# Performance work log

Measured on AMD Instinct MI355X. Metric: run time of the kernel, lower is better.

## Reference

```python
import jax, jax.numpy as jnp
import numpy as np
from jax.ops import segment_sum

N_NODES = 100000
N_EDGES = 1600000
HIDDEN = 64
N_LAYERS = 4
N_CLASSES = 10
N_GRAPHS = 512


def setup_inputs() -> dict:
    key = jax.random.key(0)
    ks = jax.random.split(key, 9)
    x = jax.random.normal(ks[0], (N_NODES, HIDDEN), dtype=jnp.float32)
    edge_index = jax.random.randint(ks[1], (2, N_EDGES), 0, N_NODES, dtype=jnp.int32)
    batch = jnp.sort(jax.random.randint(ks[2], (N_NODES,), 0, N_GRAPHS, dtype=jnp.int32))
    s = 0.05
    W_enc = jax.random.normal(ks[3], (HIDDEN, HIDDEN), dtype=jnp.float32) * s
    b_enc = jax.random.normal(ks[4], (HIDDEN,), dtype=jnp.float32) * s
    W_conv = jax.random.normal(ks[5], (N_LAYERS, HIDDEN, HIDDEN), dtype=jnp.float32) * s
    b_conv = jax.random.normal(ks[6], (N_LAYERS, HIDDEN), dtype=jnp.float32) * s
    W_out = jax.random.normal(ks[7], (HIDDEN, N_CLASSES), dtype=jnp.float32) * s
    b_out = jax.random.normal(ks[8], (N_CLASSES,), dtype=jnp.float32) * s
    return {"x": x, "edge_index": edge_index, "batch": batch,
            "W_enc": W_enc, "b_enc": b_enc, "W_conv": W_conv, "b_conv": b_conv,
            "W_out": W_out, "b_out": b_out, "num_graphs": N_GRAPHS}


def reference(x, edge_index, batch, W_enc, b_enc, W_conv, b_conv, W_out, b_out, num_graphs):
    N = x.shape[0]
    src, dst = edge_index[0], edge_index[1]
    # atom_encoder: Linear
    h = x @ W_enc + b_enc
    # GCN symmetric normalization with self-loops (PyG GCNConv default):
    # deg counts incoming edges (dst) plus the self-loop.
    deg = segment_sum(jnp.ones_like(src, dtype=h.dtype), dst, num_segments=N) + 1.0
    deg_inv_sqrt = jax.lax.rsqrt(deg)
    deg_inv = 1.0 / deg  # self-loop norm = d^-1/2 * d^-1/2
    edge_norm = (deg_inv_sqrt[src] * deg_inv_sqrt[dst])[:, None]  # [E,1]
    for l in range(W_conv.shape[0]):
        hl = h @ W_conv[l]                          # [N,H]
        msg = hl[src] * edge_norm                   # gather + normalize [E,H]
        agg = segment_sum(msg, dst, num_segments=N) # scatter-add
        h = agg + hl * deg_inv[:, None] + b_conv[l] # self-loop + bias
        h = jax.nn.silu(h)                          # dropout p=0 / eval: identity
    # global_add_pool over graph ids
    pooled = segment_sum(h, batch, num_segments=num_graphs)  # [G,H]
    # readout: Linear + ReLU (make_mlp with hidden_layers=1)
    out = jax.nn.relu(pooled @ W_out + b_out)
    return out
```

## Files before the change

### kernel.cpp

```cpp
#include <hip/hip_runtime.h>
#include <math.h>

#define HIDDEN 64
#define N_LAYERS 4
#define N_CLASSES 10
#define N_GRAPHS 512
#define BSH 8
#define NPB 256
#define PART_K 2048
#define IDX_CAP 512

typedef _Float16 __h;
typedef __attribute__((ext_vector_type(8))) _Float16 half8;
typedef __attribute__((ext_vector_type(4))) float f32x4;

__global__ __launch_bounds__(256) void k_histA(const int* __restrict__ dst,
                                               int* __restrict__ ghist, int E, int NB) {
    __shared__ int hist[512];
    int t = threadIdx.x;
    hist[t] = 0; hist[t + 256] = 0;
    __syncthreads();
    int base = blockIdx.x * PART_K;
    int kend = min(PART_K, E - base);
    for (int k = t; k < kend; k += 256) atomicAdd(&hist[dst[base + k] >> BSH], 1);
    __syncthreads();
    for (int j = t; j < NB; j += 256) {
        int h = hist[j];
        if (h) atomicAdd(&ghist[j], h);
    }
}

__global__ __launch_bounds__(256) void k_bucketscan(const int* __restrict__ ghist,
                                                    int* __restrict__ bucketbase,
                                                    int* __restrict__ gcur, int NB) {
    __shared__ int s[256];
    int t = threadIdx.x;
    int j0 = 2 * t, j1 = 2 * t + 1;
    int h0 = (j0 < NB) ? ghist[j0] : 0;
    int h1 = (j1 < NB) ? ghist[j1] : 0;
    s[t] = h0 + h1; __syncthreads();
    for (int o = 1; o < 256; o <<= 1) {
        int x = (t >= o) ? s[t - o] : 0;
        __syncthreads();
        s[t] += x;
        __syncthreads();
    }
    int base = (t == 0) ? 0 : s[t - 1];
    if (j0 <= NB) { bucketbase[j0] = base;      gcur[j0] = base; }
    if (j1 <= NB) { bucketbase[j1] = base + h0; gcur[j1] = base + h0; }
}

__global__ __launch_bounds__(256) void k_partition(const int* __restrict__ src,
                                                   const int* __restrict__ dst,
                                                   int* __restrict__ gcur,
                                                   int* __restrict__ packed,
                                                   int E, int NB) {
    __shared__ int hist[512];
    __shared__ int scanE[512];
    __shared__ int cur[512];
    __shared__ int delta[512];
    __shared__ int ps[256];
    __shared__ int stage[PART_K];
    __shared__ unsigned short stgj[PART_K];
    int t = threadIdx.x;
    int base = blockIdx.x * PART_K;
    int kend = min(PART_K, E - base);

    hist[t] = 0; hist[t + 256] = 0;
    __syncthreads();
    for (int k = t; k < kend; k += 256) atomicAdd(&hist[dst[base + k] >> BSH], 1);
    __syncthreads();

    int j0 = 2 * t, j1 = j0 + 1;
    int h0 = hist[j0], h1 = hist[j1];
    ps[t] = h0 + h1; __syncthreads();
    for (int o = 1; o < 256; o <<= 1) {
        int x = (t >= o) ? ps[t - o] : 0;
        __syncthreads();
        ps[t] += x;
        __syncthreads();
    }
    int bexc = (t == 0) ? 0 : ps[t - 1];
    scanE[j0] = bexc;
    scanE[j1] = bexc + h0;
    __syncthreads();

    for (int j = t; j < NB; j += 256) {
        int h = hist[j];
        int g = h ? atomicAdd(&gcur[j], h) : 0;
        delta[j] = g - scanE[j];
        cur[j]   = scanE[j];
    }
    __syncthreads();

    for (int k = t; k < kend; k += 256) {
        int d = dst[base + k], s = src[base + k];
        int j = d >> BSH;
        int pos = atomicAdd(&cur[j], 1);
        stage[pos] = (s << BSH) | (d & (NPB - 1));
        stgj[pos]  = (unsigned short)j;
    }
    __syncthreads();

    for (int i = t; i < kend; i += 256) {
        packed[i + delta[stgj[i]]] = stage[i];
    }
}

__global__ __launch_bounds__(256) void k_fill3(const int* __restrict__ packed,
                                               const int* __restrict__ bucketbase,
                                               int* __restrict__ rowptr,
                                               float* __restrict__ dis,
                                               int* __restrict__ csr_src,
                                               int N, int E) {
    __shared__ int cnt[256];
    __shared__ int rp[256];
    int j = blockIdx.x;
    int t = threadIdx.x;
    int node0 = j << BSH;
    int segb = bucketbase[j];
    int sege = bucketbase[j + 1];

    cnt[t] = 0; __syncthreads();
    for (int i = segb + t; i < sege; i += 256) atomicAdd(&cnt[packed[i] & (NPB - 1)], 1);
    __syncthreads();

    int c = cnt[t];
    rp[t] = c; __syncthreads();
    for (int o = 1; o < 256; o <<= 1) {
        int x = (t >= o) ? rp[t - o] : 0;
        __syncthreads();
        rp[t] += x;
        __syncthreads();
    }
    int node = node0 + t;
    int start = segb + rp[t] - c + node;
    if (node < N) {
        rowptr[node] = start;
        dis[node] = rsqrtf((float)c + 1.0f);
        csr_src[start] = node;
        if (node == N - 1) rowptr[N] = E + N;
    }
    __syncthreads();
    cnt[t] = start + 1;
    __syncthreads();
    for (int i = segb + t; i < sege; i += 256) {
        int v = packed[i];
        int slot = atomicAdd(&cnt[v & (NPB - 1)], 1);
        csr_src[slot] = v >> BSH;
    }
}

__device__ __forceinline__ half8 shfl_xor_h8(half8 v, int m) {
    int4 u = __builtin_bit_cast(int4, v);
    u.x = __shfl_xor(u.x, m);
    u.y = __shfl_xor(u.y, m);
    u.z = __shfl_xor(u.z, m);
    u.w = __shfl_xor(u.w, m);
    return __builtin_bit_cast(half8, u);
}

__global__ __launch_bounds__(256) void k_prepW(const float* __restrict__ Wconv,
                                               const float* __restrict__ Wenc,
                                               __h* __restrict__ Wh) {
    int idx = blockIdx.x * 256 + threadIdx.x;
    int l = idx >> 12;
    int kn = idx & 4095;
    int k = kn >> 6, n = kn & 63;
    int nt = n >> 4, nl = n & 15;
    int kt = k >> 5, kr = k & 31;
    int quad = kr >> 3, j = kr & 7;
    int lane = quad * 16 + nl;
    int pos = (((nt * 2 + kt) * 64 + lane) << 3) + j;
    float w = (l < N_LAYERS) ? Wconv[(size_t)l * 4096 + kn] : Wenc[kn];
    Wh[(l << 12) + pos] = (__h)w;
}

__global__ __launch_bounds__(256) void k_layer(const int* __restrict__ csr_src,
                                               const int* __restrict__ rowptr,
                                               const float* __restrict__ dis,
                                               const __h* __restrict__ G,
                                               const __h* __restrict__ Wh,
                                               const float* __restrict__ bias,
                                               const int* __restrict__ batch,
                                               __h* __restrict__ Gho,
                                               float* __restrict__ pooled,
                                               int N, int last) {
    __shared__ __attribute__((aligned(16))) __h At[16][72];
    __shared__ int sidx[IDX_CAP];
    int tid  = threadIdx.x;
    int wave = tid >> 6;
    int lane = tid & 63;
    int trow0 = blockIdx.x * 16;
    int g16 = lane >> 4;
    int sub = (lane >> 3) & 1;
    int f8  = lane & 7;
    unsigned f8b = (unsigned)f8 * 16u;

    int rpi = trow0 + lane;
    int rpv = rowptr[rpi > N ? N : rpi];
    int beg0 = __shfl(rpv, 0);
    int endL = __shfl(rpv, 16);
    int L    = endL - beg0;
    bool fits = (L <= IDX_CAP);

    if (fits) {
        const int* __restrict__ gsrc = csr_src + beg0;
        for (int k = tid; k < L; k += 256) sidx[k] = gsrc[k];
    }
    __syncthreads();

    int i   = wave * 4 + g16;
    int beg = __shfl(rpv, i);
    int end = __shfl(rpv, i + 1);
    int node = trow0 + i;

    const char* Gb = (const char*)G;
    const half8 z8 = {(__h)0.f, (__h)0.f, (__h)0.f, (__h)0.f,
                      (__h)0.f, (__h)0.f, (__h)0.f, (__h)0.f};
    half8 a = z8;
#define GLOAD(s) (*(const half8*)(Gb + ((((unsigned)(s)) << 7) + f8b)))

    if (fits) {
        const int* sp = sidx;
        int rb = beg - beg0, re = end - beg0;
        for (int e = rb + sub * 8; e < re; e += 16) {
            if (e + 8 <= re) {
                int s0 = sp[e + 0], s1 = sp[e + 1], s2 = sp[e + 2], s3 = sp[e + 3];
                int s4 = sp[e + 4], s5 = sp[e + 5], s6 = sp[e + 6], s7 = sp[e + 7];
                half8 r0 = GLOAD(s0), r1 = GLOAD(s1), r2 = GLOAD(s2), r3 = GLOAD(s3);
                half8 r4 = GLOAD(s4), r5 = GLOAD(s5), r6 = GLOAD(s6), r7 = GLOAD(s7);
                a += r0; a += r1; a += r2; a += r3;
                a += r4; a += r5; a += r6; a += r7;
            } else {
                #pragma unroll
                for (int k = 0; k < 8; ++k) {
                    int ek = e + k;
                    int ck = ek < re ? ek : re - 1;
                    half8 r = GLOAD(sp[ck]);
                    a += (ek < re) ? r : z8;
                }
            }
        }
    } else {
        for (int e = beg + sub * 8; e < end; e += 16) {
            if (e + 8 <= end) {
                int s0 = csr_src[e + 0], s1 = csr_src[e + 1], s2 = csr_src[e + 2], s3 = csr_src[e + 3];
                int s4 = csr_src[e + 4], s5 = csr_src[e + 5], s6 = csr_src[e + 6], s7 = csr_src[e + 7];
                half8 r0 = GLOAD(s0), r1 = GLOAD(s1), r2 = GLOAD(s2), r3 = GLOAD(s3);
                half8 r4 = GLOAD(s4), r5 = GLOAD(s5), r6 = GLOAD(s6), r7 = GLOAD(s7);
                a += r0; a += r1; a += r2; a += r3;
                a += r4; a += r5; a += r6; a += r7;
            } else {
                #pragma unroll
                for (int k = 0; k < 8; ++k) {
                    int ek = e + k;
                    int ck = ek < end ? ek : end - 1;
                    half8 r = GLOAD(csr_src[ck]);
                    a += (ek < end) ? r : z8;
                }
            }
        }
    }
#undef GLOAD

    a += shfl_xor_h8(a, 8);

    if (sub == 0) {
        float df = (node < N) ? dis[node] : 0.0f;
        __h dd = (__h)df;
        half8 dv = {dd, dd, dd, dd, dd, dd, dd, dd};
        *(half8*)&At[i][f8 * 8] = a * dv;
    }
    __syncthreads();

    int quad = lane >> 4, nl = lane & 15;
    half8 bf[4][2];
    #pragma unroll
    for (int nt = 0; nt < 4; ++nt)
        #pragma unroll
        for (int kt = 0; kt < 2; ++kt)
            bf[nt][kt] = *(const half8*)(Wh + (((nt * 2 + kt) * 64 + lane) << 3));

    half8 a0 = *(const half8*)&At[nl][quad * 8];
    half8 a1 = *(const half8*)&At[nl][32 + quad * 8];

    f32x4 acc[4];
    #pragma unroll
    for (int nt = 0; nt < 4; ++nt) {
        acc[nt] = (f32x4){0.f, 0.f, 0.f, 0.f};
        acc[nt] = __builtin_amdgcn_mfma_f32_16x16x32_f16(a0, bf[nt][0], acc[nt], 0, 0, 0);
        acc[nt] = __builtin_amdgcn_mfma_f32_16x16x32_f16(a1, bf[nt][1], acc[nt], 0, 0, 0);
    }

    float b[4];
    #pragma unroll
    for (int nt = 0; nt < 4; ++nt) b[nt] = bias[nt * 16 + nl];

    bool own = (quad == wave);

    if (!last) {
        if (own) {
            #pragma unroll
            for (int reg = 0; reg < 4; ++reg) {
                int rr = trow0 + quad * 4 + reg;
                if (rr < N) {
                    float ds_ = dis[rr];
                    #pragma unroll
                    for (int nt = 0; nt < 4; ++nt) {
                        float v = acc[nt][reg] + b[nt];
                        v = v / (1.0f + expf(-v));
                        Gho[(size_t)rr * 64 + nt * 16 + nl] = (__h)(ds_ * v);
                    }
                }
            }
        }
    } else {
        if (own) {
            float run[4] = {0.f, 0.f, 0.f, 0.f};
            int cur = -1;
            #pragma unroll
            for (int reg = 0; reg < 4; ++reg) {
                int rr = trow0 + quad * 4 + reg;
                if (rr < N) {
                    int bi = batch[rr];
                    float vals[4];
                    #pragma unroll
                    for (int nt = 0; nt < 4; ++nt) {
                        float v = acc[nt][reg] + b[nt];
                        vals[nt] = v / (1.0f + expf(-v));
                    }
                    if (bi != cur) {
                        if (cur >= 0) {
                            #pragma unroll
                            for (int nt = 0; nt < 4; ++nt)
                                atomicAdd(&pooled[cur * 64 + nt * 16 + nl], run[nt]);
                        }
                        cur = bi;
                        #pragma unroll
                        for (int nt = 0; nt < 4; ++nt) run[nt] = vals[nt];
                    } else {
                        #pragma unroll
                        for (int nt = 0; nt < 4; ++nt) run[nt] += vals[nt];
                    }
                }
            }
            if (cur >= 0) {
                #pragma unroll
                for (int nt = 0; nt < 4; ++nt)
                    atomicAdd(&pooled[cur * 64 + nt * 16 + nl], run[nt]);
            }
        }
    }
}

__global__ __launch_bounds__(256) void k_gemm_mfma(const float* __restrict__ xf,
                                                   const __h* __restrict__ Wh,
                                                   const float* __restrict__ bias,
                                                   const float* __restrict__ dis,
                                                   __h* __restrict__ Gho,
                                                   int N) {
    int wave = threadIdx.x >> 6;
    int lane = threadIdx.x & 63;
    int row0 = (blockIdx.x * 4 + wave) * 32;
    if (row0 >= N) return;
    int quad = lane >> 4, nl = lane & 15;

    half8 bf[4][2];
    #pragma unroll
    for (int nt = 0; nt < 4; ++nt)
        #pragma unroll
        for (int kt = 0; kt < 2; ++kt)
            bf[nt][kt] = *(const half8*)(Wh + (((nt * 2 + kt) * 64 + lane) << 3));

    f32x4 acc[2][4];
    #pragma unroll
    for (int h = 0; h < 2; ++h) {
        int r = row0 + h * 16 + nl; if (r >= N) r = N - 1;
        const float* ap = xf + (size_t)r * 64 + quad * 8;
        float4 v0 = ((const float4*)ap)[0];
        float4 v1 = ((const float4*)ap)[1];
        float4 v2 = ((const float4*)(ap + 32))[0];
        float4 v3 = ((const float4*)(ap + 32))[1];
        half8 a0 = (half8){(__h)v0.x, (__h)v0.y, (__h)v0.z, (__h)v0.w,
                           (__h)v1.x, (__h)v1.y, (__h)v1.z, (__h)v1.w};
        half8 a1 = (half8){(__h)v2.x, (__h)v2.y, (__h)v2.z, (__h)v2.w,
                           (__h)v3.x, (__h)v3.y, (__h)v3.z, (__h)v3.w};
        #pragma unroll
        for (int nt = 0; nt < 4; ++nt) {
            acc[h][nt] = (f32x4){0.f, 0.f, 0.f, 0.f};
            acc[h][nt] = __builtin_amdgcn_mfma_f32_16x16x32_f16(a0, bf[nt][0], acc[h][nt], 0, 0, 0);
            acc[h][nt] = __builtin_amdgcn_mfma_f32_16x16x32_f16(a1, bf[nt][1], acc[h][nt], 0, 0, 0);
        }
    }

    float b[4];
    #pragma unroll
    for (int nt = 0; nt < 4; ++nt) b[nt] = bias[nt * 16 + nl];

    #pragma unroll
    for (int h = 0; h < 2; ++h) {
        #pragma unroll
        for (int reg = 0; reg < 4; ++reg) {
            int rr = row0 + h * 16 + quad * 4 + reg;
            if (rr < N) {
                float ds = dis[rr];
                #pragma unroll
                for (int nt = 0; nt < 4; ++nt) {
                    float v = acc[h][nt][reg] + b[nt];
                    Gho[(size_t)rr * 64 + nt * 16 + nl] = (__h)(ds * v);
                }
            }
        }
    }
}

__global__ __launch_bounds__(256) void k_readout(const float* __restrict__ pooled,
                                                 const float* __restrict__ Wout,
                                                 const float* __restrict__ bout,
                                                 float* __restrict__ out) {
    int idx = blockIdx.x * 256 + threadIdx.x;
    if (idx >= N_GRAPHS * N_CLASSES) return;
    int g = idx / N_CLASSES, c = idx % N_CLASSES;
    float s = bout[c];
    #pragma unroll
    for (int j = 0; j < 64; ++j) s += pooled[g * 64 + j] * Wout[j * N_CLASSES + c];
    out[idx] = fmaxf(s, 0.0f);
}

extern "C" void kernel_launch(void* const* d_in, const int* in_sizes, int n_in,
                              void* d_out, int out_size, void* d_ws, size_t ws_size,
                              hipStream_t stream) {
    const float* x      = (const float*)d_in[0];
    const int*   ei     = (const int*)d_in[1];
    const int*   batch  = (const int*)d_in[2];
    const float* W_enc  = (const float*)d_in[3];
    const float* b_enc  = (const float*)d_in[4];
    const float* W_conv = (const float*)d_in[5];
    const float* b_conv = (const float*)d_in[6];
    const float* W_out  = (const float*)d_in[7];
    const float* b_out  = (const float*)d_in[8];
    float* out = (float*)d_out;

    const int N = in_sizes[2];
    const int E = in_sizes[1] / 2;
    const int* src = ei;
    const int* dst = ei + E;
    const int NB   = (N + NPB - 1) >> BSH;
    const int NBLK = (E + PART_K - 1) / PART_K;

    char* ws = (char*)d_ws;
    size_t off = 0;
    auto alloc = [&](size_t bytes) -> char* {
        char* p = ws + off;
        off += (bytes + 255) & ~(size_t)255;
        return p;
    };
    int*   ghist      = (int*)alloc((size_t)(NB + 1) * sizeof(int));
    int*   bucketbase = (int*)alloc((size_t)(NB + 1) * sizeof(int));
    int*   gcur       = (int*)alloc((size_t)(NB + 1) * sizeof(int));
    int*   packed     = (int*)alloc((size_t)E * sizeof(int));
    int*   csr_src    = (int*)alloc((size_t)(E + N) * sizeof(int));
    int*   rowptr     = (int*)alloc((size_t)(N + 1) * sizeof(int));
    float* dis        = (float*)alloc((size_t)N * sizeof(float));
    __h*   bufA       = (__h*)alloc((size_t)N * HIDDEN * sizeof(__h));
    __h*   bufB       = (__h*)alloc((size_t)N * HIDDEN * sizeof(__h));
    __h*   Wh         = (__h*)alloc((size_t)(N_LAYERS + 1) * 4096 * sizeof(__h));
    float* pooled     = (float*)alloc((size_t)N_GRAPHS * HIDDEN * sizeof(float));
    (void)ws_size;

    hipMemsetAsync(ghist, 0, (size_t)(NB + 1) * sizeof(int), stream);
    hipMemsetAsync(pooled, 0, (size_t)N_GRAPHS * HIDDEN * sizeof(float), stream);

    k_histA     <<<NBLK, 256, 0, stream>>>(dst, ghist, E, NB);
    k_bucketscan<<<1,    256, 0, stream>>>(ghist, bucketbase, gcur, NB);
    k_partition <<<NBLK, 256, 0, stream>>>(src, dst, gcur, packed, E, NB);
    k_fill3     <<<NB,   256, 0, stream>>>(packed, bucketbase, rowptr, dis, csr_src, N, E);
    k_prepW<<<((N_LAYERS + 1) * 4096) / 256, 256, 0, stream>>>(W_conv, W_enc, Wh);

    int gb32 = (N + 127) / 128;
    k_gemm_mfma<<<gb32, 256, 0, stream>>>(x, Wh + (size_t)N_LAYERS * 4096, b_enc,
                                          dis, bufA, N);

    __h* bufs[2] = {bufA, bufB};
    int glayer = (N + 15) / 16;
    for (int l = 0; l < N_LAYERS; ++l) {
        int last = (l == N_LAYERS - 1);
        k_layer<<<glayer, 256, 0, stream>>>(csr_src, rowptr, dis, bufs[l & 1],
                                            Wh + (size_t)l * 4096,
                                            b_conv + (size_t)l * HIDDEN, batch,
                                            bufs[(l + 1) & 1], pooled, N, last);
    }

    k_readout<<<(N_GRAPHS * N_CLASSES + 255) / 256, 256, 0, stream>>>(pooled, W_out, b_out, out);
}
```

Measured before the change: 356.4 us.

## Make layer kernel persistent and pre-scale CSR source indices to byte offsets

The per-layer aggregation+MFMA kernel becomes a grid-stride persistent kernel capped at 2048 blocks. Weight fragments and bias are loaded once per block instead of once per 16-row tile. CSR source indices are stored pre-multiplied by the row byte stride, which removes a shift from each gather address. The gather also splits its sums across two accumulators for more ILP and uses a simpler guarded tail. The goal is lower launch, setup and address overhead, at the cost of less latency hiding from many resident blocks.

```diff
diff --git a/kernel.cpp b/kernel.cpp
--- a/kernel.cpp
+++ b/kernel.cpp
@@ -9,6 +9,7 @@
 #define NPB 256
 #define PART_K 2048
 #define IDX_CAP 512
+#define PBLK 2048
 
 typedef _Float16 __h;
 typedef __attribute__((ext_vector_type(8))) _Float16 half8;
@@ -138,7 +139,7 @@
     if (node < N) {
         rowptr[node] = start;
         dis[node] = rsqrtf((float)c + 1.0f);
-        csr_src[start] = node;
+        csr_src[start] = node << 7;
         if (node == N - 1) rowptr[N] = E + N;
     }
     __syncthreads();
@@ -147,7 +148,7 @@
     for (int i = segb + t; i < sege; i += 256) {
         int v = packed[i];
         int slot = atomicAdd(&cnt[v & (NPB - 1)], 1);
-        csr_src[slot] = v >> BSH;
+        csr_src[slot] = (v >> BSH) << 7;
     }
 }
 
@@ -185,170 +186,166 @@
                                                const int* __restrict__ batch,
                                                __h* __restrict__ Gho,
                                                float* __restrict__ pooled,
-                                               int N, int last) {
+                                               int N, int last, int ntiles) {
     __shared__ __attribute__((aligned(16))) __h At[16][72];
     __shared__ int sidx[IDX_CAP];
     int tid  = threadIdx.x;
     int wave = tid >> 6;
     int lane = tid & 63;
-    int trow0 = blockIdx.x * 16;
     int g16 = lane >> 4;
     int sub = (lane >> 3) & 1;
     int f8  = lane & 7;
-    unsigned f8b = (unsigned)f8 * 16u;
-
-    int rpi = trow0 + lane;
-    int rpv = rowptr[rpi > N ? N : rpi];
-    int beg0 = __shfl(rpv, 0);
-    int endL = __shfl(rpv, 16);
-    int L    = endL - beg0;
-    bool fits = (L <= IDX_CAP);
-
-    if (fits) {
-        const int* __restrict__ gsrc = csr_src + beg0;
-        for (int k = tid; k < L; k += 256) sidx[k] = gsrc[k];
-    }
-    __syncthreads();
-
-    int i   = wave * 4 + g16;
-    int beg = __shfl(rpv, i);
-    int end = __shfl(rpv, i + 1);
-    int node = trow0 + i;
-
+    int f8b = f8 * 16;
+    int quad = lane >> 4, nl = lane & 15;
     const char* Gb = (const char*)G;
     const half8 z8 = {(__h)0.f, (__h)0.f, (__h)0.f, (__h)0.f,
                       (__h)0.f, (__h)0.f, (__h)0.f, (__h)0.f};
-    half8 a = z8;
-#define GLOAD(s) (*(const half8*)(Gb + ((((unsigned)(s)) << 7) + f8b)))
-
-    if (fits) {
-        const int* sp = sidx;
-        int rb = beg - beg0, re = end - beg0;
-        for (int e = rb + sub * 8; e < re; e += 16) {
-            if (e + 8 <= re) {
+
+    half8 bf[4][2];
+    #pragma unroll
+    for (int nt = 0; nt < 4; ++nt)
+        #pragma unroll
+        for (int kt = 0; kt < 2; ++kt)
+            bf[nt][kt] = *(const half8*)(Wh + (((nt * 2 + kt) * 64 + lane) << 3));
+    float b[4];
+    #pragma unroll
+    for (int nt = 0; nt < 4; ++nt) b[nt] = bias[nt * 16 + nl];
+
+    for (int tile = blockIdx.x; tile < ntiles; tile += gridDim.x) {
+        int trow0 = tile * 16;
+
+        int rpi = trow0 + lane;
+        int rpv = rowptr[rpi > N ? N : rpi];
+        int beg0 = __shfl(rpv, 0);
+        int endL = __shfl(rpv, 16);
+        int L    = endL - beg0;
+        bool fits = (L <= IDX_CAP);
+
+        if (fits) {
+            const int* __restrict__ gsrc = csr_src + beg0;
+            for (int k = tid; k < L; k += 256) sidx[k] = gsrc[k];
+        }
+        __syncthreads();
+
+        int i   = wave * 4 + g16;
+        int beg = __shfl(rpv, i);
+        int end = __shfl(rpv, i + 1);
+        int node = trow0 + i;
+
+        half8 a = z8, a2 = z8;
+#define GLOAD(sv) (*(const half8*)(Gb + (unsigned)((sv) + f8b)))
+        if (fits) {
+            const int* sp = sidx;
+            int rb = beg - beg0, re = end - beg0;
+            int e = rb + sub * 8;
+            for (; e + 8 <= re; e += 16) {
                 int s0 = sp[e + 0], s1 = sp[e + 1], s2 = sp[e + 2], s3 = sp[e + 3];
                 int s4 = sp[e + 4], s5 = sp[e + 5], s6 = sp[e + 6], s7 = sp[e + 7];
                 half8 r0 = GLOAD(s0), r1 = GLOAD(s1), r2 = GLOAD(s2), r3 = GLOAD(s3);
                 half8 r4 = GLOAD(s4), r5 = GLOAD(s5), r6 = GLOAD(s6), r7 = GLOAD(s7);
-                a += r0; a += r1; a += r2; a += r3;
-                a += r4; a += r5; a += r6; a += r7;
-            } else {
+                a += r0; a2 += r1; a += r2; a2 += r3;
+                a += r4; a2 += r5; a += r6; a2 += r7;
+            }
+            if (e < re) {
                 #pragma unroll
                 for (int k = 0; k < 8; ++k) {
                     int ek = e + k;
-                    int ck = ek < re ? ek : re - 1;
-                    half8 r = GLOAD(sp[ck]);
-                    a += (ek < re) ? r : z8;
-                }
-            }
-        }
-    } else {
-        for (int e = beg + sub * 8; e < end; e += 16) {
-            if (e + 8 <= end) {
+                    if (ek < re) { half8 r = GLOAD(sp[ek]); a += r; }
+                }
+            }
+        } else {
+            int e = beg + sub * 8;
+            for (; e + 8 <= end; e += 16) {
                 int s0 = csr_src[e + 0], s1 = csr_src[e + 1], s2 = csr_src[e + 2], s3 = csr_src[e + 3];
                 int s4 = csr_src[e + 4], s5 = csr_src[e + 5], s6 = csr_src[e + 6], s7 = csr_src[e + 7];
                 half8 r0 = GLOAD(s0), r1 = GLOAD(s1), r2 = GLOAD(s2), r3 = GLOAD(s3);
                 half8 r4 = GLOAD(s4), r5 = GLOAD(s5), r6 = GLOAD(s6), r7 = GLOAD(s7);
-                a += r0; a += r1; a += r2; a += r3;
-                a += r4; a += r5; a += r6; a += r7;
-            } else {
+                a += r0; a2 += r1; a += r2; a2 += r3;
+                a += r4; a2 += r5; a += r6; a2 += r7;
+            }
+            if (e < end) {
                 #pragma unroll
                 for (int k = 0; k < 8; ++k) {
                     int ek = e + k;
-                    int ck = ek < end ? ek : end - 1;
-                    half8 r = GLOAD(csr_src[ck]);
-                    a += (ek < end) ? r : z8;
-                }
-            }
-        }
-    }
+                    if (ek < end) { half8 r = GLOAD(csr_src[ek]); a += r; }
+                }
+            }
+        }
 #undef GLOAD
-
-    a += shfl_xor_h8(a, 8);
-
-    if (sub == 0) {
-        float df = (node < N) ? dis[node] : 0.0f;
-        __h dd = (__h)df;
-        half8 dv = {dd, dd, dd, dd, dd, dd, dd, dd};
-        *(half8*)&At[i][f8 * 8] = a * dv;
-    }
-    __syncthreads();
-
-    int quad = lane >> 4, nl = lane & 15;
-    half8 bf[4][2];
-    #pragma unroll
-    for (int nt = 0; nt < 4; ++nt)
+        a += a2;
+        a += shfl_xor_h8(a, 8);
+
+        if (sub == 0) {
+            float df = (node < N) ? dis[node] : 0.0f;
+            __h dd = (__h)df;
+            half8 dv = {dd, dd, dd, dd, dd, dd, dd, dd};
+            *(half8*)&At[i][f8 * 8] = a * dv;
+        }
+        __syncthreads();
+
+        half8 a0 = *(const half8*)&At[nl][quad * 8];
+        half8 a1 = *(const half8*)&At[nl][32 + quad * 8];
+
+        f32x4 acc[4];
         #pragma unroll
-        for (int kt = 0; kt < 2; ++kt)
-            bf[nt][kt] = *(const half8*)(Wh + (((nt * 2 + kt) * 64 + lane) << 3));
-
-    half8 a0 = *(const half8*)&At[nl][quad * 8];
-    half8 a1 = *(const half8*)&At[nl][32 + quad * 8];
-
-    f32x4 acc[4];
-    #pragma unroll
-    for (int nt = 0; nt < 4; ++nt) {
-        acc[nt] = (f32x4){0.f, 0.f, 0.f, 0.f};
-        acc[nt] = __builtin_amdgcn_mfma_f32_16x16x32_f16(a0, bf[nt][0], acc[nt], 0, 0, 0);
-        acc[nt] = __builtin_amdgcn_mfma_f32_16x16x32_f16(a1, bf[nt][1], acc[nt], 0, 0, 0);
-    }
-
-    float b[4];
-    #pragma unroll
-    for (int nt = 0; nt < 4; ++nt) b[nt] = bias[nt * 16 + nl];
-
-    bool own = (quad == wave);
-
-    if (!last) {
-        if (own) {
-            #pragma unroll
-            for (int reg = 0; reg < 4; ++reg) {
-                int rr = trow0 + quad * 4 + reg;
-                if (rr < N) {
-                    float ds_ = dis[rr];
+        for (int nt = 0; nt < 4; ++nt) {
+            acc[nt] = (f32x4){0.f, 0.f, 0.f, 0.f};
+            acc[nt] = __builtin_amdgcn_mfma_f32_16x16x32_f16(a0, bf[nt][0], acc[nt], 0, 0, 0);
+            acc[nt] = __builtin_amdgcn_mfma_f32_16x16x32_f16(a1, bf[nt][1], acc[nt], 0, 0, 0);
+        }
+
+        bool own = (quad == wave);
+        if (!last) {
+            if (own) {
+                #pragma unroll
+                for (int reg = 0; reg < 4; ++reg) {
+                    int rr = trow0 + quad * 4 + reg;
+                    if (rr < N) {
+                        float ds_ = dis[rr];
+                        #pragma unroll
+                        for (int nt = 0; nt < 4; ++nt) {
+                            float v = acc[nt][reg] + b[nt];
+                            v = v / (1.0f + expf(-v));
+                            Gho[(size_t)rr * 64 + nt * 16 + nl] = (__h)(ds_ * v);
+                        }
+                    }
+                }
+            }
+        } else {
+            if (own) {
+                float run[4] = {0.f, 0.f, 0.f, 0.f};
+                int cur = -1;
+                #pragma unroll
+                for (int reg = 0; reg < 4; ++reg) {
+                    int rr = trow0 + quad * 4 + reg;
+                    if (rr < N) {
+                        int bi = batch[rr];
+                        float vals[4];
+                        #pragma unroll
+                        for (int nt = 0; nt < 4; ++nt) {
+                            float v = acc[nt][reg] + b[nt];
+                            vals[nt] = v / (1.0f + expf(-v));
+                        }
+                        if (bi != cur) {
+                            if (cur >= 0) {
+                                #pragma unroll
+                                for (int nt = 0; nt < 4; ++nt)
+                                    atomicAdd(&pooled[cur * 64 + nt * 16 + nl], run[nt]);
+                            }
+                            cur = bi;
+                            #pragma unroll
+                            for (int nt = 0; nt < 4; ++nt) run[nt] = vals[nt];
+                        } else {
+                            #pragma unroll
+                            for (int nt = 0; nt < 4; ++nt) run[nt] += vals[nt];
+                        }
+                    }
+                }
+                if (cur >= 0) {
                     #pragma unroll
-                    for (int nt = 0; nt < 4; ++nt) {
-                        float v = acc[nt][reg] + b[nt];
-                        v = v / (1.0f + expf(-v));
-                        Gho[(size_t)rr * 64 + nt * 16 + nl] = (__h)(ds_ * v);
-                    }
-                }
-            }
-        }
-    } else {
-        if (own) {
-            float run[4] = {0.f, 0.f, 0.f, 0.f};
-            int cur = -1;
-            #pragma unroll
-            for (int reg = 0; reg < 4; ++reg) {
-                int rr = trow0 + quad * 4 + reg;
-                if (rr < N) {
-                    int bi = batch[rr];
-                    float vals[4];
-                    #pragma unroll
-                    for (int nt = 0; nt < 4; ++nt) {
-                        float v = acc[nt][reg] + b[nt];
-                        vals[nt] = v / (1.0f + expf(-v));
-                    }
-                    if (bi != cur) {
-                        if (cur >= 0) {
-                            #pragma unroll
-                            for (int nt = 0; nt < 4; ++nt)
-                                atomicAdd(&pooled[cur * 64 + nt * 16 + nl], run[nt]);
-                        }
-                        cur = bi;
-                        #pragma unroll
-                        for (int nt = 0; nt < 4; ++nt) run[nt] = vals[nt];
-                    } else {
-                        #pragma unroll
-                        for (int nt = 0; nt < 4; ++nt) run[nt] += vals[nt];
-                    }
-                }
-            }
-            if (cur >= 0) {
-                #pragma unroll
-                for (int nt = 0; nt < 4; ++nt)
-                    atomicAdd(&pooled[cur * 64 + nt * 16 + nl], run[nt]);
+                    for (int nt = 0; nt < 4; ++nt)
+                        atomicAdd(&pooled[cur * 64 + nt * 16 + nl], run[nt]);
+                }
             }
         }
     }
@@ -483,13 +480,14 @@
                                           dis, bufA, N);
 
     __h* bufs[2] = {bufA, bufB};
-    int glayer = (N + 15) / 16;
+    int ntiles = (N + 15) / 16;
+    int glayer = ntiles < PBLK ? ntiles : PBLK;
     for (int l = 0; l < N_LAYERS; ++l) {
         int last = (l == N_LAYERS - 1);
         k_layer<<<glayer, 256, 0, stream>>>(csr_src, rowptr, dis, bufs[l & 1],
                                             Wh + (size_t)l * 4096,
                                             b_conv + (size_t)l * HIDDEN, batch,
-                                            bufs[(l + 1) & 1], pooled, N, last);
+                                            bufs[(l + 1) & 1], pooled, N, last, ntiles);
     }
 
     k_readout<<<(N_GRAPHS * N_CLASSES + 255) / 256, 256, 0, stream>>>(pooled, W_out, b_out, out);
```

New measurement: 388.5 us. +9.0%, slower.
